# Optimization experiments

Measured on AMD Instinct MI355X. Metric: run time of the kernel, lower is better.

Reference implementation:

```python
import math
import jax, jax.numpy as jnp
import numpy as np

B, L, D, K = 4, 1024, 256, 64
PI = np.float32(math.pi)


def setup_inputs() -> dict:
    key = jax.random.key(0)
    ks = jax.random.split(key, 16)
    s = 0.05
    return {
        "x": jax.random.normal(ks[0], (B, L, D), jnp.float32),
        "pos_phases": jax.random.normal(ks[1], (L, K), jnp.float32) * PI,
        "W1": jax.random.normal(ks[2], (D, D), jnp.float32) * s,
        "b1": jnp.zeros((D,), jnp.float32),
        "W2": jax.random.normal(ks[3], (D, K), jnp.float32) * s,
        "b2": jnp.zeros((K,), jnp.float32),
        "Wa": jax.random.normal(ks[4], (D, K), jnp.float32) * s,
        "ba": jnp.zeros((K,), jnp.float32),
        "Wv": jax.random.normal(ks[5], (D, D), jnp.float32) * s,
        "bv": jnp.zeros((D,), jnp.float32),
        "ln_g": jnp.ones((D,), jnp.float32),
        "ln_b": jnp.zeros((D,), jnp.float32),
        "Wo": jax.random.normal(ks[6], (D, D), jnp.float32) * s,
        "bo": jnp.zeros((D,), jnp.float32),
    }


def reference(x, pos_phases, W1, b1, W2, b2, Wa, ba, Wv, bv, ln_g, ln_b, Wo, bo):
    b, l, d = x.shape
    k = Wa.shape[1]
    # content phase encoder: Linear -> GELU(exact) -> Linear, then tanh * pi
    h = jax.nn.gelu(x @ W1 + b1, approximate=False)
    content_phase = jnp.tanh(h @ W2 + b2) * PI                      # (B,L,K)
    phase = pos_phases[None, :l] + content_phase                    # (B,L,K)
    amp = jax.nn.softplus(x @ Wa + ba) + 0.1                        # (B,L,K)
    # phasor = amp * exp(i*phase), kept as real/imag parts
    pr = amp * jnp.cos(phase)
    pim = amp * jnp.sin(phase)
    V = x @ Wv + bv                                                 # (B,L,D)
    # bound = phasor[...,None] * V[...,None,:]; cumsum over L
    mr = jnp.cumsum(pr[..., None] * V[..., None, :], axis=1)        # (B,L,K,D)
    mi = jnp.cumsum(pim[..., None] * V[..., None, :], axis=1)       # (B,L,K,D)
    # Re(memory * conj(phasor)) summed over K
    retrieved = (jnp.einsum('blkd,blk->bld', mr, pr)
                 + jnp.einsum('blkd,blk->bld', mi, pim))            # (B,L,D)
    positions = jnp.arange(1, l + 1, dtype=x.dtype)
    norm = jnp.sqrt(positions * k)[None, :, None]
    r = retrieved / norm
    # to_out: LayerNorm then Linear
    mu = jnp.mean(r, axis=-1, keepdims=True)
    var = jnp.var(r, axis=-1, keepdims=True)
    rn = (r - mu) * jax.lax.rsqrt(var + 1e-5) * ln_g + ln_b
    return x + (rn @ Wo + bo)
```

## Files before the change

kernel.cpp:

```cpp
#include <hip/hip_runtime.h>
#include <hip/hip_bf16.h>
#include <math.h>

#define BB 4
#define LL 1024
#define DD 256
#define KK 64
#define NN (BB*LL)

typedef __attribute__((ext_vector_type(8))) short short8;
typedef __attribute__((ext_vector_type(4))) float f32x4;

__device__ __forceinline__ short f2bs(float f){
    union { __hip_bfloat16 h; short s; } u;
    u.h = __float2bfloat16(f);
    return u.s;
}

__global__ __launch_bounds__(256)
void prep_kernel(const float* __restrict__ x,
                 const float* __restrict__ W1, const float* __restrict__ Wv,
                 const float* __restrict__ Wo, const float* __restrict__ W2,
                 const float* __restrict__ Wa,
                 short* __restrict__ xb,
                 short* __restrict__ W1t, short* __restrict__ Wvt,
                 short* __restrict__ Wot, short* __restrict__ W2t,
                 short* __restrict__ Wat)
{
    int o = blockIdx.x * 256 + threadIdx.x;
    if (o < NN*DD){
        xb[o] = f2bs(x[o]);
        return;
    }
    o -= NN*DD;
    if (o < 3*DD*DD){
        int m = o / (DD*DD);
        int e = o - m*DD*DD;
        int n = e >> 8, k = e & 255;
        const float* src = (m==0) ? W1 : (m==1) ? Wv : Wo;
        short* dst = (m==0) ? W1t : (m==1) ? Wvt : Wot;
        dst[n*DD + k] = f2bs(src[k*DD + n]);
        return;
    }
    o -= 3*DD*DD;
    int m = o >> 14;
    int e = o & 16383;
    int n = e >> 8, k = e & 255;
    const float* src = (m==0) ? W2 : Wa;
    short* dst = (m==0) ? W2t : Wat;
    dst[n*DD + k] = f2bs(src[k*KK + n]);
}

__global__ __launch_bounds__(256)
void encode_kernel(const short* __restrict__ xb, const float* __restrict__ pos,
                   const short* __restrict__ W1t, const short* __restrict__ Wvt,
                   const short* __restrict__ W2t, const short* __restrict__ Wat,
                   const float* __restrict__ b1, const float* __restrict__ bv,
                   const float* __restrict__ b2, const float* __restrict__ ba,
                   short* __restrict__ Pb, short* __restrict__ Vt)
{
    const int t = threadIdx.x;
    const int w = t >> 6, lane = t & 63;
    const int m16 = lane & 15, quad = lane >> 4;
    const int tok0 = blockIdx.x * 16;
    const int bsel = tok0 >> 10;
    const int l0   = tok0 & 1023;

    __shared__ __align__(16) short hsb[16][264];
    __shared__ __align__(16) short vsb[16][264];

    short8 aX[8];
    {
        const short* xr = xb + (size_t)(tok0 + m16)*DD + quad*8;
        #pragma unroll
        for (int kk = 0; kk < 8; kk++) aX[kk] = *(const short8*)(xr + kk*32);
    }

    f32x4 accH[4], accV[4];
    #pragma unroll
    for (int i = 0; i < 4; i++){ accH[i] = (f32x4){0,0,0,0}; accV[i] = (f32x4){0,0,0,0}; }
    #pragma unroll
    for (int kk = 0; kk < 8; kk++){
        const short* p1 = W1t + (size_t)(w*64 + m16)*DD + kk*32 + quad*8;
        const short* pv = Wvt + (size_t)(w*64 + m16)*DD + kk*32 + quad*8;
        #pragma unroll
        for (int ns = 0; ns < 4; ns++){
            accH[ns] = __builtin_amdgcn_mfma_f32_16x16x32_bf16(
                           aX[kk], *(const short8*)(p1 + ns*16*DD), accH[ns], 0,0,0);
            accV[ns] = __builtin_amdgcn_mfma_f32_16x16x32_bf16(
                           aX[kk], *(const short8*)(pv + ns*16*DD), accV[ns], 0,0,0);
        }
    }
    #pragma unroll
    for (int ns = 0; ns < 4; ns++){
        int col = w*64 + ns*16 + m16;
        float bb1 = b1[col], bbv = bv[col];
        #pragma unroll
        for (int r2 = 0; r2 < 4; r2++){
            int row = quad*4 + r2;
            float hx = accH[ns][r2] + bb1;
            hsb[row][col] = f2bs(0.5f*hx*(1.0f + erff(hx*0.70710678118f)));
            vsb[row][col] = f2bs(accV[ns][r2] + bbv);
        }
    }
    __syncthreads();

    {
        short8 v0, v1;
        #pragma unroll
        for (int r = 0; r < 8; r++) v0[r] = vsb[r][t];
        #pragma unroll
        for (int r = 0; r < 8; r++) v1[r] = vsb[8+r][t];
        short* dst = Vt + (((size_t)bsel*256 + t) << 10) + l0;
        *(short8*)dst = v0;
        *(short8*)(dst + 8) = v1;
    }

    f32x4 accT = (f32x4){0,0,0,0}, accA = (f32x4){0,0,0,0};
    {
        const short* p2 = W2t + (size_t)(w*16 + m16)*DD + quad*8;
        const short* pa = Wat + (size_t)(w*16 + m16)*DD + quad*8;
        #pragma unroll
        for (int kk = 0; kk < 8; kk++){
            short8 aH = *(const short8*)&hsb[m16][kk*32 + quad*8];
            accT = __builtin_amdgcn_mfma_f32_16x16x32_bf16(
                       aH, *(const short8*)(p2 + kk*32), accT, 0,0,0);
            accA = __builtin_amdgcn_mfma_f32_16x16x32_bf16(
                       aX[kk], *(const short8*)(pa + kk*32), accA, 0,0,0);
        }
    }
    const int k = w*16 + m16;
    float bb2 = b2[k], bba = ba[k];
    const float PI_ = 3.14159265358979323846f;
    #pragma unroll
    for (int r2 = 0; r2 < 4; r2++){
        int tok = tok0 + quad*4 + r2;
        float cp = tanhf(accT[r2] + bb2) * PI_;
        float ph = cp + pos[(tok & (LL-1))*KK + k];
        float za = accA[r2] + bba;
        float amp = ((za > 20.f) ? za : log1pf(expf(za))) + 0.1f;
        float sn, cs;
        sincosf(ph, &sn, &cs);
        Pb[(size_t)tok*128 + k]      = f2bs(amp*cs);
        Pb[(size_t)tok*128 + 64 + k] = f2bs(amp*sn);
    }
}

__global__ __launch_bounds__(256)
void mix_kernel(const short* __restrict__ Pb, const short* __restrict__ Vt,
                float* __restrict__ R)
{
    const int t    = threadIdx.x;
    const int bb   = blockIdx.x >> 4;
    const int T    = blockIdx.x & 15;
    const int cs   = blockIdx.y * 256;
    if (cs > T*64) return;

    const int w    = t >> 6;
    const int lane = t & 63;
    const int m16  = lane & 15;
    const int quad = lane >> 4;
    const int mrow0 = T*64 + w*16;

    __shared__ __align__(16) short sP[64][136];
    __shared__ __align__(16) short sV[256][72];
    __shared__ __align__(16) short sS[4][16][72];

    f32x4 accO[16];
    #pragma unroll
    for (int i = 0; i < 16; i++) accO[i] = (f32x4){0.f,0.f,0.f,0.f};

    const short* PbB = Pb + (size_t)bb * 1024 * 128;
    const short* VtB = Vt + (size_t)bb * 256 * 1024;

    short8 aP[4];
    {
        const short* ar = PbB + (size_t)(mrow0 + m16) * 128 + quad*8;
        #pragma unroll
        for (int kk = 0; kk < 4; kk++) aP[kk] = *(const short8*)(ar + kk*32);
    }

    const int cend = min(cs + 192, T*64);
    for (int c0 = cs; c0 <= cend; c0 += 64){
        __syncthreads();
        {
            int j = t >> 2, seg = t & 3;
            const short* src = PbB + (size_t)(c0 + j)*128 + seg*32;
            #pragma unroll
            for (int q = 0; q < 4; q++)
                *(short8*)&sP[j][seg*32 + q*8] = *(const short8*)(src + q*8);
        }
        {
            int seg = t & 7;
            #pragma unroll
            for (int pass = 0; pass < 8; pass++){
                int d = pass*32 + (t >> 3);
                *(short8*)&sV[d][seg*8] =
                    *(const short8*)(VtB + (size_t)d*1024 + c0 + seg*8);
            }
        }
        __syncthreads();

        f32x4 accS[4];
        #pragma unroll
        for (int n = 0; n < 4; n++) accS[n] = (f32x4){0.f,0.f,0.f,0.f};
        #pragma unroll
        for (int ns = 0; ns < 4; ns++){
            #pragma unroll
            for (int kk = 0; kk < 4; kk++){
                short8 bP = *(const short8*)&sP[ns*16 + m16][kk*32 + quad*8];
                accS[ns] = __builtin_amdgcn_mfma_f32_16x16x32_bf16(
                               aP[kk], bP, accS[ns], 0, 0, 0);
            }
        }
        if (c0 == T*64){
            #pragma unroll
            for (int ns = 0; ns < 4; ns++){
                int ccol = c0 + ns*16 + m16;
                #pragma unroll
                for (int r2 = 0; r2 < 4; r2++){
                    int rrow = mrow0 + quad*4 + r2;
                    float v = (ccol <= rrow) ? accS[ns][r2] : 0.f;
                    sS[w][quad*4 + r2][ns*16 + m16] = f2bs(v);
                }
            }
        } else {
            #pragma unroll
            for (int ns = 0; ns < 4; ns++)
                #pragma unroll
                for (int r2 = 0; r2 < 4; r2++)
                    sS[w][quad*4 + r2][ns*16 + m16] = f2bs(accS[ns][r2]);
        }
        short8 aS0 = *(const short8*)&sS[w][m16][quad*8];
        short8 aS1 = *(const short8*)&sS[w][m16][32 + quad*8];
        #pragma unroll
        for (int ns = 0; ns < 16; ns++){
            short8 b0  = *(const short8*)&sV[ns*16 + m16][quad*8];
            short8 b1v = *(const short8*)&sV[ns*16 + m16][32 + quad*8];
            accO[ns] = __builtin_amdgcn_mfma_f32_16x16x32_bf16(aS0, b0,  accO[ns], 0,0,0);
            accO[ns] = __builtin_amdgcn_mfma_f32_16x16x32_bf16(aS1, b1v, accO[ns], 0,0,0);
        }
    }

    float* Rb = R + (size_t)bb * 1024 * 256;
    #pragma unroll
    for (int ns = 0; ns < 16; ns++){
        #pragma unroll
        for (int r2 = 0; r2 < 4; r2++){
            int rrow = mrow0 + quad*4 + r2;
            atomicAdd(&Rb[(size_t)rrow*256 + ns*16 + m16], accO[ns][r2]);
        }
    }
}

__global__ __launch_bounds__(256)
void out_kernel(const float* __restrict__ R, const float* __restrict__ x,
                const float* __restrict__ ln_g, const float* __restrict__ ln_b,
                const short* __restrict__ Wot, const float* __restrict__ bo,
                float* __restrict__ out)
{
    const int t = threadIdx.x;
    const int w = t >> 6, lane = t & 63;
    const int m16 = lane & 15, quad = lane >> 4;
    const int tok0 = blockIdx.x * 16;

    __shared__ float rs[16][DD];
    __shared__ __align__(16) short rnb[16][264];
    __shared__ float stats[16][2];

    for (int i = t; i < 16*DD; i += 256){
        int r = i >> 8;
        int l = (tok0 + r) & (LL-1);
        rs[r][i&255] = R[(size_t)tok0*DD + i] * rsqrtf((float)(l+1) * (float)KK);
    }
    __syncthreads();

    #pragma unroll
    for (int rr = 0; rr < 4; rr++){
        int r = w*4 + rr;
        float s = 0.f, ss = 0.f;
        #pragma unroll
        for (int q = 0; q < 4; q++){
            float v = rs[r][q*64 + lane];
            s += v; ss += v*v;
        }
        for (int off = 32; off; off >>= 1){
            s  += __shfl_down(s, off);
            ss += __shfl_down(ss, off);
        }
        if (lane == 0){
            float mu = s * (1.0f/DD);
            float var = ss * (1.0f/DD) - mu*mu;
            stats[r][0] = mu;
            stats[r][1] = rsqrtf(var + 1e-5f);
        }
    }
    __syncthreads();

    for (int i = t; i < 16*DD; i += 256){
        int r = i >> 8, c = i & 255;
        rnb[r][c] = f2bs((rs[r][c] - stats[r][0]) * stats[r][1] * ln_g[c] + ln_b[c]);
    }
    __syncthreads();

    f32x4 acc[4];
    #pragma unroll
    for (int i = 0; i < 4; i++) acc[i] = (f32x4){0,0,0,0};
    #pragma unroll
    for (int kk = 0; kk < 8; kk++){
        short8 aR = *(const short8*)&rnb[m16][kk*32 + quad*8];
        const short* po = Wot + (size_t)(w*64 + m16)*DD + kk*32 + quad*8;
        #pragma unroll
        for (int ns = 0; ns < 4; ns++)
            acc[ns] = __builtin_amdgcn_mfma_f32_16x16x32_bf16(
                          aR, *(const short8*)(po + ns*16*DD), acc[ns], 0,0,0);
    }
    #pragma unroll
    for (int ns = 0; ns < 4; ns++){
        int col = w*64 + ns*16 + m16;
        float bbo = bo[col];
        #pragma unroll
        for (int r2 = 0; r2 < 4; r2++){
            size_t idx = (size_t)(tok0 + quad*4 + r2)*DD + col;
            out[idx] = x[idx] + acc[ns][r2] + bbo;
        }
    }
}

extern "C" void kernel_launch(void* const* d_in, const int* in_sizes, int n_in,
                              void* d_out, int out_size, void* d_ws, size_t ws_size,
                              hipStream_t stream) {
    const float* x    = (const float*)d_in[0];
    const float* pos  = (const float*)d_in[1];
    const float* W1   = (const float*)d_in[2];
    const float* b1   = (const float*)d_in[3];
    const float* W2   = (const float*)d_in[4];
    const float* b2_  = (const float*)d_in[5];
    const float* Wa   = (const float*)d_in[6];
    const float* ba   = (const float*)d_in[7];
    const float* Wv   = (const float*)d_in[8];
    const float* bv   = (const float*)d_in[9];
    const float* ln_g = (const float*)d_in[10];
    const float* ln_b = (const float*)d_in[11];
    const float* Wo   = (const float*)d_in[12];
    const float* bo   = (const float*)d_in[13];

    float* R   = (float*)d_ws;
    short* Pb  = (short*)(R + (size_t)NN*DD);
    short* Vt  = Pb  + (size_t)NN*128;
    short* xb  = Vt  + (size_t)NN*256;
    short* W1t = xb  + (size_t)NN*256;
    short* Wvt = W1t + DD*DD;
    short* Wot = Wvt + DD*DD;
    short* W2t = Wot + DD*DD;
    short* Wat = W2t + KK*DD;

    hipMemsetAsync(R, 0, (size_t)NN*DD*sizeof(float), stream);

    const int prep_n = NN*DD + 3*DD*DD + 2*KK*DD;
    prep_kernel<<<(prep_n + 255)/256, 256, 0, stream>>>(
        x, W1, Wv, Wo, W2, Wa, xb, W1t, Wvt, Wot, W2t, Wat);

    encode_kernel<<<NN/16, 256, 0, stream>>>(xb, pos, W1t, Wvt, W2t, Wat,
                                             b1, bv, b2_, ba, Pb, Vt);
    dim3 mixgrid(BB*16, 4);
    mix_kernel<<<mixgrid, 256, 0, stream>>>(Pb, Vt, R);
    out_kernel<<<NN/16, 256, 0, stream>>>(R, x, ln_g, ln_b, Wot, bo,
                                          (float*)d_out);
}
```

Before: 130.6 us.

## Split encode into LDS-tiled gemm1 and gemm2 kernels, fold memset into prep

```diff
diff --git a/kernel.cpp b/kernel.cpp
--- a/kernel.cpp
+++ b/kernel.cpp
@@ -9,6 +9,7 @@
 #define NN (BB*LL)
 
 typedef __attribute__((ext_vector_type(8))) short short8;
+typedef __attribute__((ext_vector_type(4))) short short4v;
 typedef __attribute__((ext_vector_type(4))) float f32x4;
 
 __device__ __forceinline__ short f2bs(float f){
@@ -25,7 +26,7 @@
                  short* __restrict__ xb,
                  short* __restrict__ W1t, short* __restrict__ Wvt,
                  short* __restrict__ Wot, short* __restrict__ W2t,
-                 short* __restrict__ Wat)
+                 short* __restrict__ Wat, float* __restrict__ R)
 {
     int o = blockIdx.x * 256 + threadIdx.x;
     if (o < NN*DD){
@@ -43,93 +44,112 @@
         return;
     }
     o -= 3*DD*DD;
-    int m = o >> 14;
-    int e = o & 16383;
-    int n = e >> 8, k = e & 255;
-    const float* src = (m==0) ? W2 : Wa;
-    short* dst = (m==0) ? W2t : Wat;
-    dst[n*DD + k] = f2bs(src[k*KK + n]);
-}
-
-__global__ __launch_bounds__(256)
-void encode_kernel(const short* __restrict__ xb, const float* __restrict__ pos,
-                   const short* __restrict__ W1t, const short* __restrict__ Wvt,
-                   const short* __restrict__ W2t, const short* __restrict__ Wat,
-                   const float* __restrict__ b1, const float* __restrict__ bv,
-                   const float* __restrict__ b2, const float* __restrict__ ba,
-                   short* __restrict__ Pb, short* __restrict__ Vt)
+    if (o < 2*KK*DD){
+        int m = o >> 14;
+        int e = o & 16383;
+        int n = e >> 8, k = e & 255;
+        const float* src = (m==0) ? W2 : Wa;
+        short* dst = (m==0) ? W2t : Wat;
+        dst[n*DD + k] = f2bs(src[k*KK + n]);
+        return;
+    }
+    o -= 2*KK*DD;
+    *(f32x4*)(R + (size_t)o*4) = (f32x4){0.f,0.f,0.f,0.f};
+}
+
+__global__ __launch_bounds__(256)
+void gemm1_kernel(const short* __restrict__ xb,
+                  const short* __restrict__ W1t, const short* __restrict__ Wvt,
+                  const float* __restrict__ b1, const float* __restrict__ bv,
+                  short* __restrict__ Hb, short* __restrict__ Vt)
+{
+    const int t = threadIdx.x;
+    const int w = t >> 6, lane = t & 63;
+    const int m16 = lane & 15, quad = lane >> 4;
+    const int tok0 = blockIdx.x * 128;
+    const int gy   = blockIdx.y;
+    const int vpath = gy >> 2;
+    const int colbase = (gy & 3) * 64;
+    const int bsel = tok0 >> 10;
+    const int lbase = tok0 & 1023;
+
+    __shared__ __align__(16) short sW[64][264];
+
+    {
+        const short* W = vpath ? Wvt : W1t;
+        for (int i = t; i < 64*32; i += 256){
+            int row = i >> 5, seg = i & 31;
+            *(short8*)&sW[row][seg*8] =
+                *(const short8*)(W + (size_t)(colbase + row)*DD + seg*8);
+        }
+    }
+    __syncthreads();
+
+    short8 bF[8];
+    #pragma unroll
+    for (int kk = 0; kk < 8; kk++)
+        bF[kk] = *(const short8*)&sW[w*16 + m16][kk*32 + quad*8];
+
+    const int col = colbase + w*16 + m16;
+    const float bias = vpath ? bv[col] : b1[col];
+
+    #pragma unroll
+    for (int mt = 0; mt < 8; mt++){
+        const int row0 = tok0 + mt*16;
+        short8 aX[8];
+        const short* xr = xb + (size_t)(row0 + m16)*DD + quad*8;
+        #pragma unroll
+        for (int kk = 0; kk < 8; kk++) aX[kk] = *(const short8*)(xr + kk*32);
+        f32x4 acc = (f32x4){0.f,0.f,0.f,0.f};
+        #pragma unroll
+        for (int kk = 0; kk < 8; kk++)
+            acc = __builtin_amdgcn_mfma_f32_16x16x32_bf16(aX[kk], bF[kk], acc, 0,0,0);
+        if (!vpath){
+            #pragma unroll
+            for (int r2 = 0; r2 < 4; r2++){
+                float hx = acc[r2] + bias;
+                Hb[(size_t)(row0 + quad*4 + r2)*DD + col] =
+                    f2bs(0.5f*hx*(1.0f + erff(hx*0.70710678118f)));
+            }
+        } else {
+            short4v v4;
+            #pragma unroll
+            for (int r2 = 0; r2 < 4; r2++) v4[r2] = f2bs(acc[r2] + bias);
+            *(short4v*)(Vt + (((size_t)bsel*256 + col) << 10)
+                           + lbase + mt*16 + quad*4) = v4;
+        }
+    }
+}
+
+__global__ __launch_bounds__(256)
+void gemm2_kernel(const short* __restrict__ Hb, const short* __restrict__ xb,
+                  const float* __restrict__ pos,
+                  const short* __restrict__ W2t, const short* __restrict__ Wat,
+                  const float* __restrict__ b2, const float* __restrict__ ba,
+                  short* __restrict__ Pb)
 {
     const int t = threadIdx.x;
     const int w = t >> 6, lane = t & 63;
     const int m16 = lane & 15, quad = lane >> 4;
     const int tok0 = blockIdx.x * 16;
-    const int bsel = tok0 >> 10;
-    const int l0   = tok0 & 1023;
-
-    __shared__ __align__(16) short hsb[16][264];
-    __shared__ __align__(16) short vsb[16][264];
-
-    short8 aX[8];
-    {
-        const short* xr = xb + (size_t)(tok0 + m16)*DD + quad*8;
-        #pragma unroll
-        for (int kk = 0; kk < 8; kk++) aX[kk] = *(const short8*)(xr + kk*32);
-    }
-
-    f32x4 accH[4], accV[4];
-    #pragma unroll
-    for (int i = 0; i < 4; i++){ accH[i] = (f32x4){0,0,0,0}; accV[i] = (f32x4){0,0,0,0}; }
-    #pragma unroll
-    for (int kk = 0; kk < 8; kk++){
-        const short* p1 = W1t + (size_t)(w*64 + m16)*DD + kk*32 + quad*8;
-        const short* pv = Wvt + (size_t)(w*64 + m16)*DD + kk*32 + quad*8;
-        #pragma unroll
-        for (int ns = 0; ns < 4; ns++){
-            accH[ns] = __builtin_amdgcn_mfma_f32_16x16x32_bf16(
-                           aX[kk], *(const short8*)(p1 + ns*16*DD), accH[ns], 0,0,0);
-            accV[ns] = __builtin_amdgcn_mfma_f32_16x16x32_bf16(
-                           aX[kk], *(const short8*)(pv + ns*16*DD), accV[ns], 0,0,0);
-        }
-    }
-    #pragma unroll
-    for (int ns = 0; ns < 4; ns++){
-        int col = w*64 + ns*16 + m16;
-        float bb1 = b1[col], bbv = bv[col];
-        #pragma unroll
-        for (int r2 = 0; r2 < 4; r2++){
-            int row = quad*4 + r2;
-            float hx = accH[ns][r2] + bb1;
-            hsb[row][col] = f2bs(0.5f*hx*(1.0f + erff(hx*0.70710678118f)));
-            vsb[row][col] = f2bs(accV[ns][r2] + bbv);
-        }
-    }
-    __syncthreads();
-
-    {
-        short8 v0, v1;
-        #pragma unroll
-        for (int r = 0; r < 8; r++) v0[r] = vsb[r][t];
-        #pragma unroll
-        for (int r = 0; r < 8; r++) v1[r] = vsb[8+r][t];
-        short* dst = Vt + (((size_t)bsel*256 + t) << 10) + l0;
-        *(short8*)dst = v0;
-        *(short8*)(dst + 8) = v1;
-    }
+    const int k = w*16 + m16;
 
     f32x4 accT = (f32x4){0,0,0,0}, accA = (f32x4){0,0,0,0};
     {
-        const short* p2 = W2t + (size_t)(w*16 + m16)*DD + quad*8;
-        const short* pa = Wat + (size_t)(w*16 + m16)*DD + quad*8;
+        const short* hr = Hb + (size_t)(tok0 + m16)*DD + quad*8;
+        const short* xr = xb + (size_t)(tok0 + m16)*DD + quad*8;
+        const short* p2 = W2t + (size_t)k*DD + quad*8;
+        const short* pa = Wat + (size_t)k*DD + quad*8;
         #pragma unroll
         for (int kk = 0; kk < 8; kk++){
-            short8 aH = *(const short8*)&hsb[m16][kk*32 + quad*8];
+            short8 aH = *(const short8*)(hr + kk*32);
+            short8 aX = *(const short8*)(xr + kk*32);
             accT = __builtin_amdgcn_mfma_f32_16x16x32_bf16(
                        aH, *(const short8*)(p2 + kk*32), accT, 0,0,0);
             accA = __builtin_amdgcn_mfma_f32_16x16x32_bf16(
-                       aX[kk], *(const short8*)(pa + kk*32), accA, 0,0,0);
-        }
-    }
-    const int k = w*16 + m16;
+                       aX, *(const short8*)(pa + kk*32), accA, 0,0,0);
+        }
+    }
     float bb2 = b2[k], bba = ba[k];
     const float PI_ = 3.14159265358979323846f;
     #pragma unroll
@@ -349,20 +369,21 @@
     short* Pb  = (short*)(R + (size_t)NN*DD);
     short* Vt  = Pb  + (size_t)NN*128;
     short* xb  = Vt  + (size_t)NN*256;
-    short* W1t = xb  + (size_t)NN*256;
+    short* Hb  = xb  + (size_t)NN*256;
+    short* W1t = Hb  + (size_t)NN*256;
     short* Wvt = W1t + DD*DD;
     short* Wot = Wvt + DD*DD;
     short* W2t = Wot + DD*DD;
     short* Wat = W2t + KK*DD;
 
-    hipMemsetAsync(R, 0, (size_t)NN*DD*sizeof(float), stream);
-
-    const int prep_n = NN*DD + 3*DD*DD + 2*KK*DD;
-    prep_kernel<<<(prep_n + 255)/256, 256, 0, stream>>>(
-        x, W1, Wv, Wo, W2, Wa, xb, W1t, Wvt, Wot, W2t, Wat);
-
-    encode_kernel<<<NN/16, 256, 0, stream>>>(xb, pos, W1t, Wvt, W2t, Wat,
-                                             b1, bv, b2_, ba, Pb, Vt);
+    const int prep_n = NN*DD + 3*DD*DD + 2*KK*DD + (NN*DD)/4;
+    prep_kernel<<<prep_n/256, 256, 0, stream>>>(
+        x, W1, Wv, Wo, W2, Wa, xb, W1t, Wvt, Wot, W2t, Wat, R);
+
+    dim3 g1grid(NN/128, 8);
+    gemm1_kernel<<<g1grid, 256, 0, stream>>>(xb, W1t, Wvt, b1, bv, Hb, Vt);
+    gemm2_kernel<<<NN/16, 256, 0, stream>>>(Hb, xb, pos, W2t, Wat, b2_, ba, Pb);
+
     dim3 mixgrid(BB*16, 4);
     mix_kernel<<<mixgrid, 256, 0, stream>>>(Pb, Vt, R);
     out_kernel<<<NN/16, 256, 0, stream>>>(R, x, ln_g, ln_b, Wot, bo,
```

Measured after the change: 134.2 us. +2.8%, slower.

## Fuse output LayerNorm+projection into mix kernel via last-block counter, fold memset into prep

Applied to the files above, without the earlier changes.

```diff
diff --git a/kernel.cpp b/kernel.cpp
--- a/kernel.cpp
+++ b/kernel.cpp
@@ -25,13 +25,11 @@
                  short* __restrict__ xb,
                  short* __restrict__ W1t, short* __restrict__ Wvt,
                  short* __restrict__ Wot, short* __restrict__ W2t,
-                 short* __restrict__ Wat)
+                 short* __restrict__ Wat, float* __restrict__ R,
+                 int* __restrict__ cnt)
 {
     int o = blockIdx.x * 256 + threadIdx.x;
-    if (o < NN*DD){
-        xb[o] = f2bs(x[o]);
-        return;
-    }
+    if (o < NN*DD){ xb[o] = f2bs(x[o]); return; }
     o -= NN*DD;
     if (o < 3*DD*DD){
         int m = o / (DD*DD);
@@ -43,12 +41,22 @@
         return;
     }
     o -= 3*DD*DD;
-    int m = o >> 14;
-    int e = o & 16383;
-    int n = e >> 8, k = e & 255;
-    const float* src = (m==0) ? W2 : Wa;
-    short* dst = (m==0) ? W2t : Wat;
-    dst[n*DD + k] = f2bs(src[k*KK + n]);
+    if (o < 2*KK*DD){
+        int m = o >> 14;
+        int e = o & 16383;
+        int n = e >> 8, k = e & 255;
+        const float* src = (m==0) ? W2 : Wa;
+        short* dst = (m==0) ? W2t : Wat;
+        dst[n*DD + k] = f2bs(src[k*KK + n]);
+        return;
+    }
+    o -= 2*KK*DD;
+    if (o < (NN*DD)/4){
+        *(f32x4*)(R + (size_t)o*4) = (f32x4){0.f,0.f,0.f,0.f};
+        return;
+    }
+    o -= (NN*DD)/4;
+    if (o < 64) cnt[o] = 0;
 }
 
 __global__ __launch_bounds__(256)
@@ -147,8 +155,12 @@
 }
 
 __global__ __launch_bounds__(256)
-void mix_kernel(const short* __restrict__ Pb, const short* __restrict__ Vt,
-                float* __restrict__ R)
+void mixout_kernel(const short* __restrict__ Pb, const short* __restrict__ Vt,
+                   float* __restrict__ R, int* __restrict__ cnt,
+                   const float* __restrict__ x,
+                   const float* __restrict__ ln_g, const float* __restrict__ ln_b,
+                   const short* __restrict__ Wot, const float* __restrict__ bo,
+                   float* __restrict__ out)
 {
     const int t    = threadIdx.x;
     const int bb   = blockIdx.x >> 4;
@@ -162,9 +174,11 @@
     const int quad = lane >> 4;
     const int mrow0 = T*64 + w*16;
 
-    __shared__ __align__(16) short sP[64][136];
-    __shared__ __align__(16) short sV[256][72];
-    __shared__ __align__(16) short sS[4][16][72];
+    __shared__ __align__(16) char smem[63488];
+    short (*sP)[136]     = (short(*)[136])smem;
+    short (*sV)[72]      = (short(*)[72])(smem + 17408);
+    short (*sS)[16][72]  = (short(*)[16][72])(smem + 54272);
+    __shared__ int isLast;
 
     f32x4 accO[16];
     #pragma unroll
@@ -251,78 +265,83 @@
             atomicAdd(&Rb[(size_t)rrow*256 + ns*16 + m16], accO[ns][r2]);
         }
     }
-}
-
-__global__ __launch_bounds__(256)
-void out_kernel(const float* __restrict__ R, const float* __restrict__ x,
-                const float* __restrict__ ln_g, const float* __restrict__ ln_b,
-                const short* __restrict__ Wot, const float* __restrict__ bo,
-                float* __restrict__ out)
-{
-    const int t = threadIdx.x;
-    const int w = t >> 6, lane = t & 63;
-    const int m16 = lane & 15, quad = lane >> 4;
-    const int tok0 = blockIdx.x * 16;
-
-    __shared__ float rs[16][DD];
-    __shared__ __align__(16) short rnb[16][264];
-    __shared__ float stats[16][2];
-
-    for (int i = t; i < 16*DD; i += 256){
-        int r = i >> 8;
-        int l = (tok0 + r) & (LL-1);
-        rs[r][i&255] = R[(size_t)tok0*DD + i] * rsqrtf((float)(l+1) * (float)KK);
-    }
+
+    __threadfence();
     __syncthreads();
-
-    #pragma unroll
-    for (int rr = 0; rr < 4; rr++){
-        int r = w*4 + rr;
-        float s = 0.f, ss = 0.f;
-        #pragma unroll
-        for (int q = 0; q < 4; q++){
-            float v = rs[r][q*64 + lane];
-            s += v; ss += v*v;
-        }
-        for (int off = 32; off; off >>= 1){
-            s  += __shfl_down(s, off);
-            ss += __shfl_down(ss, off);
-        }
-        if (lane == 0){
-            float mu = s * (1.0f/DD);
-            float var = ss * (1.0f/DD) - mu*mu;
-            stats[r][0] = mu;
-            stats[r][1] = rsqrtf(var + 1e-5f);
-        }
+    if (t == 0){
+        int nparts = (T >> 2) + 1;
+        int old = atomicAdd(&cnt[bb*16 + T], 1);
+        isLast = (old == nparts - 1);
     }
     __syncthreads();
-
-    for (int i = t; i < 16*DD; i += 256){
-        int r = i >> 8, c = i & 255;
-        rnb[r][c] = f2bs((rs[r][c] - stats[r][0]) * stats[r][1] * ln_g[c] + ln_b[c]);
-    }
-    __syncthreads();
-
-    f32x4 acc[4];
-    #pragma unroll
-    for (int i = 0; i < 4; i++) acc[i] = (f32x4){0,0,0,0};
-    #pragma unroll
-    for (int kk = 0; kk < 8; kk++){
-        short8 aR = *(const short8*)&rnb[m16][kk*32 + quad*8];
-        const short* po = Wot + (size_t)(w*64 + m16)*DD + kk*32 + quad*8;
-        #pragma unroll
-        for (int ns = 0; ns < 4; ns++)
-            acc[ns] = __builtin_amdgcn_mfma_f32_16x16x32_bf16(
-                          aR, *(const short8*)(po + ns*16*DD), acc[ns], 0,0,0);
-    }
-    #pragma unroll
-    for (int ns = 0; ns < 4; ns++){
-        int col = w*64 + ns*16 + m16;
-        float bbo = bo[col];
-        #pragma unroll
-        for (int r2 = 0; r2 < 4; r2++){
-            size_t idx = (size_t)(tok0 + quad*4 + r2)*DD + col;
-            out[idx] = x[idx] + acc[ns][r2] + bbo;
+    if (!isLast) return;
+    __threadfence();
+
+    float (*rs)[DD]    = (float(*)[DD])smem;
+    short (*rnb)[264]  = (short(*)[264])(smem + 16384);
+    float (*stats)[2]  = (float(*)[2])(smem + 24832);
+
+    for (int sub = 0; sub < 4; sub++){
+        const int tok0 = bb*1024 + T*64 + sub*16;
+        __syncthreads();
+        for (int i = t; i < 16*DD; i += 256){
+            int r = i >> 8;
+            int l = (tok0 + r) & (LL-1);
+            float v = __hip_atomic_load(&R[(size_t)tok0*DD + i],
+                                        __ATOMIC_RELAXED, __HIP_MEMORY_SCOPE_AGENT);
+            rs[r][i&255] = v * rsqrtf((float)(l+1) * (float)KK);
+        }
+        __syncthreads();
+
+        #pragma unroll
+        for (int rr = 0; rr < 4; rr++){
+            int r = w*4 + rr;
+            float s = 0.f, ss = 0.f;
+            #pragma unroll
+            for (int q = 0; q < 4; q++){
+                float v = rs[r][q*64 + lane];
+                s += v; ss += v*v;
+            }
+            for (int off = 32; off; off >>= 1){
+                s  += __shfl_down(s, off);
+                ss += __shfl_down(ss, off);
+            }
+            if (lane == 0){
+                float mu = s * (1.0f/DD);
+                float var = ss * (1.0f/DD) - mu*mu;
+                stats[r][0] = mu;
+                stats[r][1] = rsqrtf(var + 1e-5f);
+            }
+        }
+        __syncthreads();
+
+        for (int i = t; i < 16*DD; i += 256){
+            int r = i >> 8, c = i & 255;
+            rnb[r][c] = f2bs((rs[r][c] - stats[r][0]) * stats[r][1] * ln_g[c] + ln_b[c]);
+        }
+        __syncthreads();
+
+        f32x4 acc[4];
+        #pragma unroll
+        for (int i = 0; i < 4; i++) acc[i] = (f32x4){0,0,0,0};
+        #pragma unroll
+        for (int kk = 0; kk < 8; kk++){
+            short8 aR = *(const short8*)&rnb[m16][kk*32 + quad*8];
+            const short* po = Wot + (size_t)(w*64 + m16)*DD + kk*32 + quad*8;
+            #pragma unroll
+            for (int ns = 0; ns < 4; ns++)
+                acc[ns] = __builtin_amdgcn_mfma_f32_16x16x32_bf16(
+                              aR, *(const short8*)(po + ns*16*DD), acc[ns], 0,0,0);
+        }
+        #pragma unroll
+        for (int ns = 0; ns < 4; ns++){
+            int col = w*64 + ns*16 + m16;
+            float bbo = bo[col];
+            #pragma unroll
+            for (int r2 = 0; r2 < 4; r2++){
+                size_t idx = (size_t)(tok0 + quad*4 + r2)*DD + col;
+                out[idx] = x[idx] + acc[ns][r2] + bbo;
+            }
         }
     }
 }
@@ -354,17 +373,17 @@
     short* Wot = Wvt + DD*DD;
     short* W2t = Wot + DD*DD;
     short* Wat = W2t + KK*DD;
-
-    hipMemsetAsync(R, 0, (size_t)NN*DD*sizeof(float), stream);
-
-    const int prep_n = NN*DD + 3*DD*DD + 2*KK*DD;
+    int*   cnt = (int*)(Wat + KK*DD);
+
+    const int prep_n = NN*DD + 3*DD*DD + 2*KK*DD + (NN*DD)/4 + 64;
     prep_kernel<<<(prep_n + 255)/256, 256, 0, stream>>>(
-        x, W1, Wv, Wo, W2, Wa, xb, W1t, Wvt, Wot, W2t, Wat);
+        x, W1, Wv, Wo, W2, Wa, xb, W1t, Wvt, Wot, W2t, Wat, R, cnt);
 
     encode_kernel<<<NN/16, 256, 0, stream>>>(xb, pos, W1t, Wvt, W2t, Wat,
                                              b1, bv, b2_, ba, Pb, Vt);
+
     dim3 mixgrid(BB*16, 4);
-    mix_kernel<<<mixgrid, 256, 0, stream>>>(Pb, Vt, R);
-    out_kernel<<<NN/16, 256, 0, stream>>>(R, x, ln_g, ln_b, Wot, bo,
-                                          (float*)d_out);
-}
+    mixout_kernel<<<mixgrid, 256, 0, stream>>>(Pb, Vt, R, cnt, x,
+                                               ln_g, ln_b, Wot, bo,
+                                               (float*)d_out);
+}
```

After: 161.5 us. 23.7% more time.

## Replace atomic fp32 accumulation with per-split bf16 partial buffers reduced in out_kernel

Applied to the files above, without the earlier changes.

```diff
diff --git a/kernel.cpp b/kernel.cpp
--- a/kernel.cpp
+++ b/kernel.cpp
@@ -15,6 +15,11 @@
     union { __hip_bfloat16 h; short s; } u;
     u.h = __float2bfloat16(f);
     return u.s;
+}
+__device__ __forceinline__ float bs2f(short s){
+    union { unsigned int u; float f; } v;
+    v.u = ((unsigned int)(unsigned short)s) << 16;
+    return v.f;
 }
 
 __global__ __launch_bounds__(256)
@@ -28,10 +33,7 @@
                  short* __restrict__ Wat)
 {
     int o = blockIdx.x * 256 + threadIdx.x;
-    if (o < NN*DD){
-        xb[o] = f2bs(x[o]);
-        return;
-    }
+    if (o < NN*DD){ xb[o] = f2bs(x[o]); return; }
     o -= NN*DD;
     if (o < 3*DD*DD){
         int m = o / (DD*DD);
@@ -43,12 +45,14 @@
         return;
     }
     o -= 3*DD*DD;
-    int m = o >> 14;
-    int e = o & 16383;
-    int n = e >> 8, k = e & 255;
-    const float* src = (m==0) ? W2 : Wa;
-    short* dst = (m==0) ? W2t : Wat;
-    dst[n*DD + k] = f2bs(src[k*KK + n]);
+    if (o < 2*KK*DD){
+        int m = o >> 14;
+        int e = o & 16383;
+        int n = e >> 8, k = e & 255;
+        const float* src = (m==0) ? W2 : Wa;
+        short* dst = (m==0) ? W2t : Wat;
+        dst[n*DD + k] = f2bs(src[k*KK + n]);
+    }
 }
 
 __global__ __launch_bounds__(256)
@@ -148,7 +152,7 @@
 
 __global__ __launch_bounds__(256)
 void mix_kernel(const short* __restrict__ Pb, const short* __restrict__ Vt,
-                float* __restrict__ R)
+                short* __restrict__ Rp)
 {
     const int t    = threadIdx.x;
     const int bb   = blockIdx.x >> 4;
@@ -162,9 +166,11 @@
     const int quad = lane >> 4;
     const int mrow0 = T*64 + w*16;
 
-    __shared__ __align__(16) short sP[64][136];
-    __shared__ __align__(16) short sV[256][72];
-    __shared__ __align__(16) short sS[4][16][72];
+    __shared__ __align__(16) char smem[63488];
+    short (*sP)[136]    = (short(*)[136])smem;
+    short (*sV)[72]     = (short(*)[72])(smem + 17408);
+    short (*sS)[16][72] = (short(*)[16][72])(smem + 54272);
+    short (*sO)[264]    = (short(*)[264])smem;
 
     f32x4 accO[16];
     #pragma unroll
@@ -242,19 +248,27 @@
         }
     }
 
-    float* Rb = R + (size_t)bb * 1024 * 256;
-    #pragma unroll
-    for (int ns = 0; ns < 16; ns++){
-        #pragma unroll
-        for (int r2 = 0; r2 < 4; r2++){
-            int rrow = mrow0 + quad*4 + r2;
-            atomicAdd(&Rb[(size_t)rrow*256 + ns*16 + m16], accO[ns][r2]);
-        }
+    __syncthreads();
+    #pragma unroll
+    for (int ns = 0; ns < 16; ns++)
+        #pragma unroll
+        for (int r2 = 0; r2 < 4; r2++)
+            sO[w*16 + quad*4 + r2][ns*16 + m16] = f2bs(accO[ns][r2]);
+    __syncthreads();
+
+    short* dst = Rp + (size_t)blockIdx.y * NN * DD
+                    + ((size_t)bb*1024 + T*64) * DD;
+    {
+        int row = t >> 2, seg = t & 3;
+        #pragma unroll
+        for (int q = 0; q < 8; q++)
+            *(short8*)(dst + (size_t)row*DD + seg*64 + q*8) =
+                *(const short8*)&sO[row][seg*64 + q*8];
     }
 }
 
 __global__ __launch_bounds__(256)
-void out_kernel(const float* __restrict__ R, const float* __restrict__ x,
+void out_kernel(const short* __restrict__ Rp, const float* __restrict__ x,
                 const float* __restrict__ ln_g, const float* __restrict__ ln_b,
                 const short* __restrict__ Wot, const float* __restrict__ bo,
                 float* __restrict__ out)
@@ -263,6 +277,7 @@
     const int w = t >> 6, lane = t & 63;
     const int m16 = lane & 15, quad = lane >> 4;
     const int tok0 = blockIdx.x * 16;
+    const int pmax = (tok0 & 1023) >> 8;
 
     __shared__ float rs[16][DD];
     __shared__ __align__(16) short rnb[16][264];
@@ -271,7 +286,10 @@
     for (int i = t; i < 16*DD; i += 256){
         int r = i >> 8;
         int l = (tok0 + r) & (LL-1);
-        rs[r][i&255] = R[(size_t)tok0*DD + i] * rsqrtf((float)(l+1) * (float)KK);
+        float s = 0.f;
+        for (int p = 0; p <= pmax; p++)
+            s += bs2f(Rp[(size_t)p*NN*DD + (size_t)tok0*DD + i]);
+        rs[r][i&255] = s * rsqrtf((float)(l+1) * (float)KK);
     }
     __syncthreads();
 
@@ -345,8 +363,8 @@
     const float* Wo   = (const float*)d_in[12];
     const float* bo   = (const float*)d_in[13];
 
-    float* R   = (float*)d_ws;
-    short* Pb  = (short*)(R + (size_t)NN*DD);
+    short* Rp  = (short*)d_ws;
+    short* Pb  = Rp  + (size_t)4*NN*DD;
     short* Vt  = Pb  + (size_t)NN*128;
     short* xb  = Vt  + (size_t)NN*256;
     short* W1t = xb  + (size_t)NN*256;
@@ -355,16 +373,15 @@
     short* W2t = Wot + DD*DD;
     short* Wat = W2t + KK*DD;
 
-    hipMemsetAsync(R, 0, (size_t)NN*DD*sizeof(float), stream);
-
     const int prep_n = NN*DD + 3*DD*DD + 2*KK*DD;
     prep_kernel<<<(prep_n + 255)/256, 256, 0, stream>>>(
         x, W1, Wv, Wo, W2, Wa, xb, W1t, Wvt, Wot, W2t, Wat);
 
     encode_kernel<<<NN/16, 256, 0, stream>>>(xb, pos, W1t, Wvt, W2t, Wat,
                                              b1, bv, b2_, ba, Pb, Vt);
+
     dim3 mixgrid(BB*16, 4);
-    mix_kernel<<<mixgrid, 256, 0, stream>>>(Pb, Vt, R);
-    out_kernel<<<NN/16, 256, 0, stream>>>(R, x, ln_g, ln_b, Wot, bo,
+    mix_kernel<<<mixgrid, 256, 0, stream>>>(Pb, Vt, Rp);
+    out_kernel<<<NN/16, 256, 0, stream>>>(Rp, x, ln_g, ln_b, Wot, bo,
                                           (float*)d_out);
 }
```

Result: slower. 139.9 us (+7.1%).
